# Optimization experiments

Measured on AMD Instinct MI355X. Metric: run time of the kernel, lower is better.

Reference implementation:

```python
import jax, jax.numpy as jnp
import numpy as np

T, B, H, K, V, O, VS, DM = 128, 256, 128, 64, 128, 512, 3, 32


def _ln(x):
    m = jnp.mean(x, -1, keepdims=True)
    v = jnp.var(x, -1, keepdims=True)
    return (x - m) / jnp.sqrt(v + 1e-5)


def setup_inputs() -> dict:
    key = jax.random.key(0)
    ks = jax.random.split(key, 16)
    n = lambda k, shape, std=0.02: jax.random.normal(k, shape, jnp.float32) * std
    return {
        "obs": jax.random.randint(ks[0], (T, B), 0, O),
        "vel": jax.random.normal(ks[1], (T, B, VS), jnp.float32),
        "exploration": jax.random.uniform(ks[2], (T, B), dtype=jnp.float32),
        "hidden_init": n(ks[3], (1, H), 0.5),
        "embed_W": n(ks[4], (O, H)),
        "vel_W": n(ks[5], (H, VS)), "vel_b": jnp.zeros((H,), jnp.float32),
        "hyp_W1": n(ks[6], (DM, VS)), "hyp_b1": jnp.zeros((DM,), jnp.float32),
        "hyp_W2": n(ks[7], (H * H, DM), 0.001), "hyp_b2": jnp.zeros((H * H,), jnp.float32),
        "gate_W": n(ks[8], (H, 2 * H)), "gate_b": jnp.zeros((H,), jnp.float32),
        "pred_W": n(ks[9], (O, H)), "pred_b": jnp.zeros((O,), jnp.float32),
        "mem_W1": n(ks[10], (200, 3)), "mem_b1": jnp.zeros((200,), jnp.float32),
        "mem_W2": n(ks[11], (1, 200)), "mem_b2": jnp.zeros((1,), jnp.float32),
        "Wqk": n(ks[12], (K, H)), "Wv": n(ks[13], (V, H)),
    }


def reference(obs, vel, exploration, hidden_init, embed_W, vel_W, vel_b,
              hyp_W1, hyp_b1, hyp_W2, hyp_b2, gate_W, gate_b, pred_W, pred_b,
              mem_W1, mem_b1, mem_W2, mem_b2, Wqk, Wv):
    i_to_h_all = embed_W[obs]                                       # [T,B,H]
    vel_emb_all = jnp.einsum('tbv,hv->tbh', vel, vel_W) + vel_b      # [T,B,H]
    hyp_h = jax.nn.silu(jnp.einsum('tbv,dv->tbd', vel, hyp_W1) + hyp_b1)  # [T,B,DM]
    h0 = jnp.tanh(jnp.tile(hidden_init, (B, 1)))                     # [B,H]
    keys0 = jnp.zeros((T, B, K), jnp.float32)
    vals0 = jnp.zeros((T, B, V), jnp.float32)
    probs0 = jnp.zeros((T, B), jnp.float32)
    scale = 1.0 / np.sqrt(K).astype(np.float32)

    def step(carry, xs):
        hidden, keys, vals, probs = carry
        i, i_to_h, hyp_t, vemb_t, expl_t = xs
        # hypernet-generated per-sample transition matrix + path integration
        Tm = (hyp_t @ hyp_W2.T + hyp_b2).reshape(B, H, H)
        pi = jnp.einsum('bij,bj->bi', Tm, hidden) + vemb_t
        pi_pred = _ln(jnp.tanh(pi))
        # external-memory dot-product attention over stored (key, value) slots
        q = pi_pred @ Wqk.T                                          # [B,K]
        scores = jnp.einsum('bk,tbk->tb', q, keys) * scale           # [T,B]
        valid = jnp.arange(T)[:, None] < i
        attn = jax.nn.softmax(jnp.where(valid, scores, -1e9), axis=0)
        has_mem = (i > 0).astype(jnp.float32)
        mem_ret = jnp.einsum('tb,tbv->bv', attn * probs, vals) * has_mem
        mem = _ln(mem_ret)
        # sigmoid-gated RNN update between generative (pi) and input paths
        gate = jax.nn.sigmoid(jnp.concatenate([pi, i_to_h], -1) @ gate_W.T + gate_b)
        hidden_new = jnp.tanh(gate * pi + (1.0 - gate) * i_to_h)
        # EM model predicts from the retrieved + normalized memory
        logits = mem @ pred_W.T + pred_b                             # [B,O]
        # write decision MLP on [max inner prod, normalized position, exploration]
        max_ip = jnp.max(jnp.where(valid, scores, -1e9), axis=0) * has_mem
        pos = jnp.full((B,), 1.0, jnp.float32) * (i.astype(jnp.float32) / T)
        feat = jnp.stack([max_ip, pos, expl_t], -1)                  # [B,3]
        h1 = jax.nn.leaky_relu(feat @ mem_W1.T + mem_b1, 0.1)
        p_write = jax.nn.sigmoid(h1 @ mem_W2.T + mem_b2)[:, 0]
        keys = keys.at[i].set(hidden_new @ Wqk.T)
        vals = vals.at[i].set(hidden_new @ Wv.T)
        probs = probs.at[i].set(p_write)
        return (hidden_new, keys, vals, probs), (logits, hidden_new, pi, gate)

    xs = (jnp.arange(T), i_to_h_all, hyp_h, vel_emb_all, exploration)
    _, (logits, inf_h, gen, gating) = jax.lax.scan(step, (h0, keys0, vals0, probs0), xs)
    preds = jax.nn.softmax(logits, axis=-1)
    return preds, logits, inf_h, gen, gating
```

## Files before the change

### kernel.cpp

```cpp
#include <hip/hip_runtime.h>

#ifndef __has_builtin
#define __has_builtin(x) 0
#endif

#define DEV static __device__ __forceinline__

#define TT 128
#define BB 256
#define HH 128
#define KK 64
#define VV 128
#define OO 512
#define JBLK 132
#define KEXT (JBLK*32)

static const size_t PRED_OFF  = 0;
static const size_t LOGIT_OFF = (size_t)TT*BB*OO;
static const size_t INFH_OFF  = LOGIT_OFF + (size_t)TT*BB*OO;
static const size_t GEN_OFF   = INFH_OFF + (size_t)TT*BB*HH;
static const size_t GATE_OFF  = GEN_OFF + (size_t)TT*BB*HH;

typedef float f32x4 __attribute__((ext_vector_type(4)));

DEV unsigned short f2bf(float x){
  unsigned int u = __float_as_uint(x);
  u = (u + 0x7fffu + ((u >> 16) & 1u)) >> 16;
  return (unsigned short)u;
}
DEV float bf2f(unsigned short v){ return __uint_as_float(((unsigned int)v) << 16); }

DEV unsigned char enc8_sw(float x){
  unsigned int u = __float_as_uint(x);
  unsigned int s = (u >> 24) & 0x80u;
  int e = (int)((u >> 23) & 0xffu) - 127;
  unsigned int m = u & 0x7fffffu;
  if (((u >> 23) & 0xffu) == 0) return (unsigned char)s;
  if (e < -10) return (unsigned char)s;
  if (e >= -6) {
    unsigned int mant = m >> 20, rem = m & 0xfffffu;
    if (rem > 0x80000u || (rem == 0x80000u && (mant & 1u))) mant++;
    unsigned int ee = (unsigned int)(e + 7);
    if (mant == 8u) { mant = 0u; ee++; }
    if (ee >= 15u) return (unsigned char)(s | 0x7Eu);
    return (unsigned char)(s | (ee << 3) | mant);
  }
  unsigned int full = 0x800000u | m;
  int sh = 20 + (-6 - e);
  unsigned int mant = full >> sh;
  unsigned int rem  = full & ((1u << sh) - 1u);
  unsigned int halfv = 1u << (sh - 1);
  if (rem > halfv || (rem == halfv && (mant & 1u))) mant++;
  if (mant >= 8u) return (unsigned char)(s | (1u << 3));
  return (unsigned char)(s | mant);
}

DEV unsigned char enc8(float v){
#if __has_builtin(__builtin_amdgcn_cvt_pk_fp8_f32)
  int r = __builtin_amdgcn_cvt_pk_fp8_f32(v, v, 0, false);
  return (unsigned char)(r & 0xff);
#else
  return enc8_sw(v);
#endif
}

DEV unsigned int pack4_fp8(float a, float b, float c, float d){
#if __has_builtin(__builtin_amdgcn_cvt_pk_fp8_f32)
  int w = __builtin_amdgcn_cvt_pk_fp8_f32(a, b, 0, false);
  w = __builtin_amdgcn_cvt_pk_fp8_f32(c, d, w, true);
  return (unsigned int)w;
#else
  return (unsigned int)enc8_sw(a) | ((unsigned int)enc8_sw(b)<<8)
       | ((unsigned int)enc8_sw(c)<<16) | ((unsigned int)enc8_sw(d)<<24);
#endif
}

#define W2_DWORDS 135168
#define GW_DWORDS 8192
__global__ __launch_bounds__(256) void k_pack(const float* __restrict__ hW2,
                                              const float* __restrict__ hb2,
                                              const float* __restrict__ gW,
                                              unsigned char* __restrict__ w2p,
                                              unsigned char* __restrict__ gwp){
  int D = blockIdx.x * 256 + threadIdx.x;
  if (D < W2_DWORDS) {
    int flat = D * 4;
    int l  = (flat >> 3) & 63;
    int w  = (flat >> 9) & 7;
    int j  = flat >> 12;
    int cb = flat & 7;
    int i  = w*16 + (l & 15);
    int db = ((l >> 4) << 3) + cb;
    unsigned int outw = 0;
    for (int cc = 0; cc < 4; ++cc) {
      int d = db + cc;
      float v;
      if (j < 128) v = hW2[((size_t)i*128 + j)*32 + d];
      else         v = hb2[(size_t)i*128 + (j-128)*32 + d];
      outw |= ((unsigned int)enc8(v * 1024.0f)) << (8*cc);
    }
    ((unsigned int*)w2p)[D] = outw;
  } else if (D < W2_DWORDS + GW_DWORDS) {
    int Dg = D - W2_DWORDS;
    int flat = Dg * 4;
    int l  = (flat >> 3) & 63;
    int w  = (flat >> 9) & 7;
    int kc = flat >> 12;
    int cb = flat & 7;
    int i  = w*16 + (l & 15);
    int k0 = kc*32 + ((l >> 4) << 3) + cb;
    unsigned int outw = 0;
    for (int cc = 0; cc < 4; ++cc)
      outw |= ((unsigned int)enc8(gW[(size_t)i*256 + k0 + cc] * 64.0f)) << (8*cc);
    ((unsigned int*)gwp)[Dg] = outw;
  }
}

struct Scan2Smem {
  unsigned long long U[JBLK*64];
  unsigned long long GW[4096];
  float h[128*17];
  float pi[128*17];
  float i2h[128*17];
  float hyps[16*32];
  float velg[64];
  float velWs[384];
  float velbs[128];
  float gbs[128];
  float hypW1s[96];
  float hypb1s[32];
};

__global__ __launch_bounds__(512) void k_scan2(
    const int* __restrict__ obs, const float* __restrict__ vel,
    const float* __restrict__ hinit, const float* __restrict__ embW,
    const float* __restrict__ velW, const float* __restrict__ velb,
    const float* __restrict__ hW1, const float* __restrict__ hb1,
    const float* __restrict__ gb,
    const unsigned char* __restrict__ w2p, const unsigned char* __restrict__ gwp,
    float* __restrict__ out)
{
  extern __shared__ char smemraw[];
  Scan2Smem* sm = (Scan2Smem*)smemraw;
  const int tid = threadIdx.x;
  const int blk = blockIdx.x;
  const int b0 = blk * 16;

  const unsigned long long* gwu = (const unsigned long long*)gwp;
  for (int idx = tid; idx < 4096; idx += 512) sm->GW[idx] = gwu[idx];
  if (tid < 384) sm->velWs[tid] = velW[tid];
  if (tid < 128) { sm->velbs[tid] = velb[tid]; sm->gbs[tid] = gb[tid]; }
  if (tid < 96)  sm->hypW1s[tid] = hW1[tid];
  if (tid < 32)  sm->hypb1s[tid] = hb1[tid];
  if (tid < 128) {
    float hv = tanhf(hinit[tid]);
    #pragma unroll
    for (int g = 0; g < 16; ++g) sm->h[tid*17+g] = hv;
  }
  __syncthreads();

  const int ln = tid & 63, wv = tid >> 6;
  const int gg = tid & 15;
  const int d0 = ((tid >> 4) & 3) << 3;
  const unsigned long long* Au = (const unsigned long long*)w2p + (size_t)wv*64 + ln;

  for (int t = 0; t < TT; ++t) {
    {
      int g2 = tid >> 5, i0 = (tid & 31) << 2;
      int ov = obs[t*BB + b0 + g2];
      float4 e = *(const float4*)&embW[(size_t)ov*HH + i0];
      sm->i2h[(i0+0)*17+g2] = e.x; sm->i2h[(i0+1)*17+g2] = e.y;
      sm->i2h[(i0+2)*17+g2] = e.z; sm->i2h[(i0+3)*17+g2] = e.w;
      int dh = tid & 31;
      const float* vp = &vel[((size_t)t*BB + b0 + g2)*3];
      float a = vp[0]*sm->hypW1s[dh*3+0] + vp[1]*sm->hypW1s[dh*3+1]
              + vp[2]*sm->hypW1s[dh*3+2] + sm->hypb1s[dh];
      sm->hyps[g2*32+dh] = a / (1.0f + __expf(-a));
      if (tid < 48) sm->velg[(tid/3)*4 + tid%3] = vel[((size_t)t*BB + b0 + tid/3)*3 + tid%3];
    }
    __syncthreads();
    {
      float hyp8[8];
      #pragma unroll
      for (int c = 0; c < 8; ++c) hyp8[c] = sm->hyps[gg*32 + d0 + c];
      #pragma unroll
      for (int it = 0; it < 17; ++it) {
        int j = wv + it*8;
        if (j < JBLK) {
          float u[8];
          if (j < 128) {
            float hv = sm->h[j*17+gg] * 32.0f;
            #pragma unroll
            for (int c = 0; c < 8; ++c) u[c] = hv * hyp8[c];
          } else {
            int jj = (j-128)*32 + d0;
            #pragma unroll
            for (int c = 0; c < 8; ++c) u[c] = sm->h[(jj+c)*17+gg] * 32.0f;
          }
          unsigned int w0 = pack4_fp8(u[0], u[1], u[2], u[3]);
          unsigned int w1 = pack4_fp8(u[4], u[5], u[6], u[7]);
          sm->U[j*64 + (tid & 63)] = ((unsigned long long)w1 << 32) | w0;
        }
      }
    }
    __syncthreads();
    {
      f32x4 a0 = {0.f,0.f,0.f,0.f}, a1 = a0, a2 = a0, a3 = a0;
      #pragma unroll 3
      for (int j4 = 0; j4 < JBLK; j4 += 4) {
        long A0 = (long)Au[(size_t)(j4+0)*512]; long B0 = (long)sm->U[(j4+0)*64 + ln];
        long A1 = (long)Au[(size_t)(j4+1)*512]; long B1 = (long)sm->U[(j4+1)*64 + ln];
        long A2 = (long)Au[(size_t)(j4+2)*512]; long B2 = (long)sm->U[(j4+2)*64 + ln];
        long A3 = (long)Au[(size_t)(j4+3)*512]; long B3 = (long)sm->U[(j4+3)*64 + ln];
        a0 = __builtin_amdgcn_mfma_f32_16x16x32_fp8_fp8(A0, B0, a0, 0, 0, 0);
        a1 = __builtin_amdgcn_mfma_f32_16x16x32_fp8_fp8(A1, B1, a1, 0, 0, 0);
        a2 = __builtin_amdgcn_mfma_f32_16x16x32_fp8_fp8(A2, B2, a2, 0, 0, 0);
        a3 = __builtin_amdgcn_mfma_f32_16x16x32_fp8_fp8(A3, B3, a3, 0, 0, 0);
      }
      f32x4 accT = (a0 + a1) + (a2 + a3);
      #pragma unroll
      for (int r = 0; r < 4; ++r) {
        int i = wv*16 + ((ln>>4)<<2) + r, g = ln & 15;
        float p = accT[r] * (1.0f/32768.0f)
                + sm->velg[g*4+0]*sm->velWs[i*3+0] + sm->velg[g*4+1]*sm->velWs[i*3+1]
                + sm->velg[g*4+2]*sm->velWs[i*3+2] + sm->velbs[i];
        sm->pi[i*17+g] = p;
      }
    }
    __syncthreads();
    {
      int kc = tid >> 6;
      int k0 = kc*32 + d0;
      float u[8];
      #pragma unroll
      for (int c = 0; c < 8; ++c) {
        int k = k0 + c;
        u[c] = (k < 128 ? sm->pi[k*17+gg] : sm->i2h[(k-128)*17+gg]) * 32.0f;
      }
      unsigned int w0 = pack4_fp8(u[0], u[1], u[2], u[3]);
      unsigned int w1 = pack4_fp8(u[4], u[5], u[6], u[7]);
      sm->U[kc*64 + (tid & 63)] = ((unsigned long long)w1 << 32) | w0;
    }
    __syncthreads();
    {
      f32x4 ga = {0.f,0.f,0.f,0.f};
      #pragma unroll
      for (int kc = 0; kc < 8; ++kc) {
        long A = (long)sm->GW[(kc*8 + wv)*64 + ln];
        long B = (long)sm->U[kc*64 + ln];
        ga = __builtin_amdgcn_mfma_f32_16x16x32_fp8_fp8(A, B, ga, 0, 0, 0);
      }
      #pragma unroll
      for (int r = 0; r < 4; ++r) {
        int i = wv*16 + ((ln>>4)<<2) + r, g = ln & 15;
        float z = ga[r] * (1.0f/2048.0f) + sm->gbs[i];
        float gt = 1.0f / (1.0f + __expf(-z));
        float pv = sm->pi[i*17+g], ih = sm->i2h[i*17+g];
        float hn = tanhf(gt*pv + (1.0f - gt)*ih);
        sm->h[i*17+g]   = hn;
        sm->i2h[i*17+g] = gt;
      }
    }
    __syncthreads();
    {
      int g2 = tid >> 5, i0 = (tid & 31) << 2;
      size_t ob = ((size_t)t*BB + b0 + g2)*HH + i0;
      float4 v;
      v.x = sm->pi[(i0+0)*17+g2]; v.y = sm->pi[(i0+1)*17+g2];
      v.z = sm->pi[(i0+2)*17+g2]; v.w = sm->pi[(i0+3)*17+g2];
      *(float4*)&out[GEN_OFF + ob] = v;
      v.x = sm->h[(i0+0)*17+g2];  v.y = sm->h[(i0+1)*17+g2];
      v.z = sm->h[(i0+2)*17+g2];  v.w = sm->h[(i0+3)*17+g2];
      *(float4*)&out[INFH_OFF + ob] = v;
      v.x = sm->i2h[(i0+0)*17+g2]; v.y = sm->i2h[(i0+1)*17+g2];
      v.z = sm->i2h[(i0+2)*17+g2]; v.w = sm->i2h[(i0+3)*17+g2];
      *(float4*)&out[GATE_OFF + ob] = v;
    }
    __syncthreads();
  }
}

struct QkvSmem {
  float wqk[64 * 132];
  float wv[128 * 132];
  float pp[132];
  float hh[132];
  float red[4];
  float stats[2];
};

__global__ __launch_bounds__(256) void k_qkv(const float* __restrict__ out,
    const float* __restrict__ Wqk, const float* __restrict__ Wv,
    float* __restrict__ qbuf, unsigned short* __restrict__ keysBF,
    unsigned short* __restrict__ valsBF)
{
  extern __shared__ char smemraw[];
  QkvSmem* sm = (QkvSmem*)smemraw;
  const int tid = threadIdx.x, b = blockIdx.x;

  for (int idx = tid; idx < 64 * 128; idx += 256) { int o = idx >> 7, j = idx & 127; sm->wqk[o * 132 + j] = Wqk[idx]; }
  for (int idx = tid; idx < 128 * 128; idx += 256) { int o = idx >> 7, j = idx & 127; sm->wv[o * 132 + j] = Wv[idx]; }
  __syncthreads();

  for (int t = 0; t < TT; ++t) {
    if (tid < 128) {
      size_t base = ((size_t)t * BB + b) * HH + tid;
      sm->hh[tid] = out[INFH_OFF + base];
      sm->pp[tid] = tanhf(out[GEN_OFF + base]);
    }
    __syncthreads();
    if (tid < 128) {
      float v = sm->pp[tid];
      float s1 = v, s2 = v * v;
      #pragma unroll
      for (int off = 32; off; off >>= 1) { s1 += __shfl_down(s1, off); s2 += __shfl_down(s2, off); }
      if ((tid & 63) == 0) { sm->red[tid >> 6] = s1; sm->red[2 + (tid >> 6)] = s2; }
    }
    __syncthreads();
    if (tid == 0) {
      float s1 = sm->red[0] + sm->red[1], s2 = sm->red[2] + sm->red[3];
      float m = s1 * (1.0f / 128.0f);
      float var = s2 * (1.0f / 128.0f) - m * m;
      sm->stats[0] = m; sm->stats[1] = rsqrtf(var + 1e-5f);
    }
    __syncthreads();
    if (tid < 128) sm->pp[tid] = (sm->pp[tid] - sm->stats[0]) * sm->stats[1];
    __syncthreads();
    {
      int o = tid;
      if (o < 64) {
        const float* wr = &sm->wqk[o * 132];
        float s = 0.f;
        #pragma unroll 8
        for (int j = 0; j < 128; j += 4) {
          float4 xv = *(const float4*)&sm->pp[j];
          float4 w4 = *(const float4*)&wr[j];
          s += xv.x * w4.x + xv.y * w4.y + xv.z * w4.z + xv.w * w4.w;
        }
        qbuf[((size_t)t * BB + b) * KK + o] = s;
      } else if (o < 128) {
        int kk = o - 64;
        const float* wr = &sm->wqk[kk * 132];
        float s = 0.f;
        #pragma unroll 8
        for (int j = 0; j < 128; j += 4) {
          float4 xv = *(const float4*)&sm->hh[j];
          float4 w4 = *(const float4*)&wr[j];
          s += xv.x * w4.x + xv.y * w4.y + xv.z * w4.z + xv.w * w4.w;
        }
        keysBF[((size_t)t * BB + b) * KK + kk] = f2bf(s);
      } else {
        int vv = o - 128;
        const float* wr = &sm->wv[vv * 132];
        float s = 0.f;
        #pragma unroll 8
        for (int j = 0; j < 128; j += 4) {
          float4 xv = *(const float4*)&sm->hh[j];
          float4 w4 = *(const float4*)&wr[j];
          s += xv.x * w4.x + xv.y * w4.y + xv.z * w4.z + xv.w * w4.w;
        }
        valsBF[((size_t)t * BB + b) * VV + vv] = f2bf(s);
      }
    }
    __syncthreads();
  }
}

struct ScoresSmem { float q[128 * 68]; };

__global__ __launch_bounds__(128) void k_scores(const float* __restrict__ qbuf,
    const unsigned short* __restrict__ keysBF, const float* __restrict__ expl,
    const float* __restrict__ mW1, const float* __restrict__ mb1,
    const float* __restrict__ mW2, const float* __restrict__ mb2,
    float* __restrict__ Sg, float* __restrict__ probs)
{
  extern __shared__ char smemraw[];
  ScoresSmem* sm = (ScoresSmem*)smemraw;
  const int tid = threadIdx.x, b = blockIdx.x;

  for (int idx = tid; idx < 128 * 64; idx += 128) {
    int tq = idx >> 6, c = idx & 63;
    sm->q[tq * 68 + c] = qbuf[((size_t)tq * BB + b) * KK + c];
  }
  float kreg[64];
  {
    const uint4* kp = (const uint4*)&keysBF[((size_t)tid * BB + b) * KK];
    #pragma unroll
    for (int qq = 0; qq < 8; ++qq) {
      uint4 kv = kp[qq];
      const unsigned short* ku = (const unsigned short*)&kv;
      #pragma unroll
      for (int c = 0; c < 8; ++c) kreg[qq * 8 + c] = bf2f(ku[c]);
    }
  }
  __syncthreads();

  float* srow = &Sg[(size_t)b * TT * TT];
  for (int tq = 0; tq < TT; ++tq) {
    float s = 0.f;
    #pragma unroll
    for (int c = 0; c < 64; c += 4) {
      float4 qv = *(const float4*)&sm->q[tq * 68 + c];
      s += qv.x * kreg[c] + qv.y * kreg[c + 1] + qv.z * kreg[c + 2] + qv.w * kreg[c + 3];
    }
    srow[(size_t)tq * TT + tid] = s * 0.125f;
  }
  __syncthreads();

  {
    int tq = tid;
    const float* r = &srow[(size_t)tq * TT];
    float mx = -3.0e38f;
    for (int tk = 0; tk < tq; ++tk) mx = fmaxf(mx, r[tk]);
    float f0 = (tq > 0) ? mx : 0.0f;
    float f1 = (float)tq * (1.0f / 128.0f);
    float f2 = expl[(size_t)tq * BB + b];
    float a = 0.f;
    for (int u = 0; u < 200; ++u) {
      float h1 = mW1[u * 3] * f0 + mW1[u * 3 + 1] * f1 + mW1[u * 3 + 2] * f2 + mb1[u];
      h1 = (h1 > 0.f) ? h1 : 0.1f * h1;
      a += mW2[u] * h1;
    }
    float p = 1.0f / (1.0f + __expf(-(a + mb2[0])));
    probs[(size_t)b * TT + tq] = p;
  }
}

struct AttnSmem {
  float w[32 * 132];
  float mem[32 * 132];
  float pw[128 * 132];
};

__global__ __launch_bounds__(256) void k_attn(const float* __restrict__ Sg,
    const float* __restrict__ probs, const unsigned short* __restrict__ valsBF,
    const float* __restrict__ pW, const float* __restrict__ pb,
    float* __restrict__ out)
{
  extern __shared__ char smemraw[];
  AttnSmem* sm = (AttnSmem*)smemraw;
  const int tid = threadIdx.x;
  const int t = blockIdx.x >> 3, g = blockIdx.x & 7;
  const int bloc = tid >> 3, s8 = tid & 7;
  const int b = g * 32 + bloc;

  float acc[16];
  #pragma unroll
  for (int c = 0; c < 16; ++c) acc[c] = 0.f;

  float inv = 0.f;
  if (t > 0) {
    const float* srow = &Sg[((size_t)b * TT + t) * TT];
    float mx = -3.0e38f;
    for (int tk = s8; tk < t; tk += 8) mx = fmaxf(mx, srow[tk]);
    #pragma unroll
    for (int off = 4; off; off >>= 1) mx = fmaxf(mx, __shfl_xor(mx, off, 8));
    float es = 0.f;
    for (int tk = s8; tk < t; tk += 8) {
      float e = __expf(srow[tk] - mx);
      es += e;
      sm->w[bloc * 132 + tk] = e * probs[(size_t)b * TT + tk];
    }
    #pragma unroll
    for (int off = 4; off; off >>= 1) es += __shfl_xor(es, off, 8);
    inv = 1.0f / es;
  }
  __syncthreads();
  if (t > 0) {
    for (int tk = 0; tk < t; ++tk) {
      float wv = sm->w[bloc * 132 + tk] * inv;
      const uint4* vp = (const uint4*)&valsBF[((size_t)tk * BB + b) * VV + s8 * 16];
      uint4 v0 = vp[0], v1 = vp[1];
      const unsigned short* u0 = (const unsigned short*)&v0;
      const unsigned short* u1 = (const unsigned short*)&v1;
      #pragma unroll
      for (int c = 0; c < 8; ++c) acc[c] += wv * bf2f(u0[c]);
      #pragma unroll
      for (int c = 0; c < 8; ++c) acc[8 + c] += wv * bf2f(u1[c]);
    }
  }
  float s1 = 0.f, s2 = 0.f;
  #pragma unroll
  for (int c = 0; c < 16; ++c) { s1 += acc[c]; s2 += acc[c] * acc[c]; }
  #pragma unroll
  for (int off = 4; off; off >>= 1) { s1 += __shfl_xor(s1, off, 8); s2 += __shfl_xor(s2, off, 8); }
  float m = s1 * (1.0f / 128.0f);
  float var = s2 * (1.0f / 128.0f) - m * m;
  float sc = rsqrtf(var + 1e-5f);
  #pragma unroll
  for (int c = 0; c < 16; ++c) sm->mem[bloc * 132 + s8 * 16 + c] = (acc[c] - m) * sc;
  __syncthreads();

  const int og = tid >> 5, bl2 = tid & 31;
  const int b2 = g * 32 + bl2;
  for (int st = 0; st < 4; ++st) {
    for (int idx = tid; idx < 128 * 128; idx += 256) {
      int o = idx >> 7, i = idx & 127;
      sm->pw[o * 132 + i] = pW[((size_t)(st * 128 + o)) * HH + i];
    }
    __syncthreads();
    #pragma unroll
    for (int ob = 0; ob < 4; ++ob) {
      int oo = og * 16 + ob * 4;
      float a0 = pb[st * 128 + oo], a1 = pb[st * 128 + oo + 1];
      float a2 = pb[st * 128 + oo + 2], a3 = pb[st * 128 + oo + 3];
      for (int i = 0; i < 128; i += 4) {
        float4 mv = *(const float4*)&sm->mem[bl2 * 132 + i];
        float4 w0 = *(const float4*)&sm->pw[(oo + 0) * 132 + i];
        float4 w1 = *(const float4*)&sm->pw[(oo + 1) * 132 + i];
        float4 w2 = *(const float4*)&sm->pw[(oo + 2) * 132 + i];
        float4 w3 = *(const float4*)&sm->pw[(oo + 3) * 132 + i];
        a0 += mv.x * w0.x + mv.y * w0.y + mv.z * w0.z + mv.w * w0.w;
        a1 += mv.x * w1.x + mv.y * w1.y + mv.z * w1.z + mv.w * w1.w;
        a2 += mv.x * w2.x + mv.y * w2.y + mv.z * w2.z + mv.w * w2.w;
        a3 += mv.x * w3.x + mv.y * w3.y + mv.z * w3.z + mv.w * w3.w;
      }
      size_t base = LOGIT_OFF + ((size_t)t * BB + b2) * OO + st * 128 + oo;
      out[base] = a0; out[base + 1] = a1; out[base + 2] = a2; out[base + 3] = a3;
    }
    __syncthreads();
  }
  {
    const float* lrow = &out[LOGIT_OFF + ((size_t)t * BB + b) * OO];
    float mx = -3.0e38f;
    for (int o = s8; o < OO; o += 8) mx = fmaxf(mx, lrow[o]);
    #pragma unroll
    for (int off = 4; off; off >>= 1) mx = fmaxf(mx, __shfl_xor(mx, off, 8));
    float zs = 0.f;
    for (int o = s8; o < OO; o += 8) zs += __expf(lrow[o] - mx);
    #pragma unroll
    for (int off = 4; off; off >>= 1) zs += __shfl_xor(zs, off, 8);
    float zi = 1.0f / zs;
    float* prow = &out[PRED_OFF + ((size_t)t * BB + b) * OO];
    for (int o = s8; o < OO; o += 8) prow[o] = __expf(lrow[o] - mx) * zi;
  }
}

extern "C" void kernel_launch(void* const* d_in, const int* in_sizes, int n_in,
                              void* d_out, int out_size, void* d_ws, size_t ws_size,
                              hipStream_t stream) {
  (void)in_sizes; (void)n_in; (void)out_size; (void)ws_size;
  const int*   obs   = (const int*)d_in[0];
  const float* vel   = (const float*)d_in[1];
  const float* expl  = (const float*)d_in[2];
  const float* hinit = (const float*)d_in[3];
  const float* embW  = (const float*)d_in[4];
  const float* velW  = (const float*)d_in[5];
  const float* velb  = (const float*)d_in[6];
  const float* hW1   = (const float*)d_in[7];
  const float* hb1   = (const float*)d_in[8];
  const float* hW2   = (const float*)d_in[9];
  const float* hb2   = (const float*)d_in[10];
  const float* gW    = (const float*)d_in[11];
  const float* gb    = (const float*)d_in[12];
  const float* pW    = (const float*)d_in[13];
  const float* pb    = (const float*)d_in[14];
  const float* mW1   = (const float*)d_in[15];
  const float* mb1   = (const float*)d_in[16];
  const float* mW2   = (const float*)d_in[17];
  const float* mb2   = (const float*)d_in[18];
  const float* Wqk   = (const float*)d_in[19];
  const float* Wv    = (const float*)d_in[20];
  float* out = (float*)d_out;
  char* ws = (char*)d_ws;

  unsigned char*  w2p    = (unsigned char*)(ws + 0);
  unsigned char*  gwp    = (unsigned char*)(ws + 589824);
  float*          qbuf   = (float*)(ws + 1048576);
  unsigned short* keysBF = (unsigned short*)(ws + 9437184);
  unsigned short* valsBF = (unsigned short*)(ws + 13631488);
  float*          Sg     = (float*)(ws + 22020096);
  float*          probs  = (float*)(ws + 38797312);

  k_pack  <<<dim3(560),  dim3(256), 0,                   stream>>>(hW2, hb2, gW, w2p, gwp);
  k_scan2 <<<dim3(16),   dim3(512), sizeof(Scan2Smem),   stream>>>(obs, vel, hinit, embW, velW, velb,
                                                                   hW1, hb1, gb, w2p, gwp, out);
  k_qkv   <<<dim3(256),  dim3(256), sizeof(QkvSmem),     stream>>>(out, Wqk, Wv, qbuf, keysBF, valsBF);
  k_scores<<<dim3(256),  dim3(128), sizeof(ScoresSmem),  stream>>>(qbuf, keysBF, expl, mW1, mb1, mW2, mb2,
                                                                   Sg, probs);
  k_attn  <<<dim3(1024), dim3(256), sizeof(AttnSmem),    stream>>>(Sg, probs, valsBF, pW, pb, out);
}
```

Measured before the change: 3.282 ms.

## Keep hypernet and gate weights resident in registers across scan steps

```diff
diff --git a/kernel.cpp b/kernel.cpp
--- a/kernel.cpp
+++ b/kernel.cpp
@@ -14,6 +14,8 @@
 #define OO 512
 #define JBLK 132
 #define KEXT (JBLK*32)
+#define NJR 64
+#define NSTR (JBLK-NJR)
 
 static const size_t PRED_OFF  = 0;
 static const size_t LOGIT_OFF = (size_t)TT*BB*OO;
@@ -116,9 +118,8 @@
   }
 }
 
-struct Scan2Smem {
+struct Scan3Smem {
   unsigned long long U[JBLK*64];
-  unsigned long long GW[4096];
   float h[128*17];
   float pi[128*17];
   float i2h[128*17];
@@ -131,7 +132,7 @@
   float hypb1s[32];
 };
 
-__global__ __launch_bounds__(512) void k_scan2(
+__global__ __launch_bounds__(512) void k_scan3(
     const int* __restrict__ obs, const float* __restrict__ vel,
     const float* __restrict__ hinit, const float* __restrict__ embW,
     const float* __restrict__ velW, const float* __restrict__ velb,
@@ -141,13 +142,11 @@
     float* __restrict__ out)
 {
   extern __shared__ char smemraw[];
-  Scan2Smem* sm = (Scan2Smem*)smemraw;
+  Scan3Smem* sm = (Scan3Smem*)smemraw;
   const int tid = threadIdx.x;
   const int blk = blockIdx.x;
   const int b0 = blk * 16;
 
-  const unsigned long long* gwu = (const unsigned long long*)gwp;
-  for (int idx = tid; idx < 4096; idx += 512) sm->GW[idx] = gwu[idx];
   if (tid < 384) sm->velWs[tid] = velW[tid];
   if (tid < 128) { sm->velbs[tid] = velb[tid]; sm->gbs[tid] = gb[tid]; }
   if (tid < 96)  sm->hypW1s[tid] = hW1[tid];
@@ -163,6 +162,14 @@
   const int gg = tid & 15;
   const int d0 = ((tid >> 4) & 3) << 3;
   const unsigned long long* Au = (const unsigned long long*)w2p + (size_t)wv*64 + ln;
+  const unsigned long long* Gu = (const unsigned long long*)gwp;
+
+  unsigned long long Areg[NJR];
+  #pragma unroll
+  for (int r = 0; r < NJR; ++r) Areg[r] = Au[(size_t)r*512];
+  unsigned long long GWreg[8];
+  #pragma unroll
+  for (int kc = 0; kc < 8; ++kc) GWreg[kc] = Gu[(size_t)(kc*8 + wv)*64 + ln];
 
   for (int t = 0; t < TT; ++t) {
     {
@@ -205,19 +212,32 @@
     }
     __syncthreads();
     {
-      f32x4 a0 = {0.f,0.f,0.f,0.f}, a1 = a0, a2 = a0, a3 = a0;
-      #pragma unroll 3
-      for (int j4 = 0; j4 < JBLK; j4 += 4) {
-        long A0 = (long)Au[(size_t)(j4+0)*512]; long B0 = (long)sm->U[(j4+0)*64 + ln];
-        long A1 = (long)Au[(size_t)(j4+1)*512]; long B1 = (long)sm->U[(j4+1)*64 + ln];
-        long A2 = (long)Au[(size_t)(j4+2)*512]; long B2 = (long)sm->U[(j4+2)*64 + ln];
-        long A3 = (long)Au[(size_t)(j4+3)*512]; long B3 = (long)sm->U[(j4+3)*64 + ln];
-        a0 = __builtin_amdgcn_mfma_f32_16x16x32_fp8_fp8(A0, B0, a0, 0, 0, 0);
-        a1 = __builtin_amdgcn_mfma_f32_16x16x32_fp8_fp8(A1, B1, a1, 0, 0, 0);
-        a2 = __builtin_amdgcn_mfma_f32_16x16x32_fp8_fp8(A2, B2, a2, 0, 0, 0);
-        a3 = __builtin_amdgcn_mfma_f32_16x16x32_fp8_fp8(A3, B3, a3, 0, 0, 0);
-      }
-      f32x4 accT = (a0 + a1) + (a2 + a3);
+      unsigned long long As[8];
+      #pragma unroll
+      for (int p = 0; p < 8; ++p) As[p] = Au[(size_t)(NJR+p)*512];
+
+      f32x4 acc[4];
+      #pragma unroll
+      for (int r = 0; r < 4; ++r) acc[r] = (f32x4){0.f,0.f,0.f,0.f};
+
+      #pragma unroll
+      for (int j4 = 0; j4 < NJR; j4 += 4) {
+        long B0 = (long)sm->U[(j4+0)*64 + ln];
+        long B1 = (long)sm->U[(j4+1)*64 + ln];
+        long B2 = (long)sm->U[(j4+2)*64 + ln];
+        long B3 = (long)sm->U[(j4+3)*64 + ln];
+        acc[0] = __builtin_amdgcn_mfma_f32_16x16x32_fp8_fp8((long)Areg[j4+0], B0, acc[0], 0, 0, 0);
+        acc[1] = __builtin_amdgcn_mfma_f32_16x16x32_fp8_fp8((long)Areg[j4+1], B1, acc[1], 0, 0, 0);
+        acc[2] = __builtin_amdgcn_mfma_f32_16x16x32_fp8_fp8((long)Areg[j4+2], B2, acc[2], 0, 0, 0);
+        acc[3] = __builtin_amdgcn_mfma_f32_16x16x32_fp8_fp8((long)Areg[j4+3], B3, acc[3], 0, 0, 0);
+      }
+      #pragma unroll
+      for (int c = 0; c < NSTR; ++c) {
+        long B = (long)sm->U[(NJR+c)*64 + ln];
+        acc[c & 3] = __builtin_amdgcn_mfma_f32_16x16x32_fp8_fp8((long)As[c & 7], B, acc[c & 3], 0, 0, 0);
+        if (c + 8 < NSTR) As[c & 7] = Au[(size_t)(NJR+c+8)*512];
+      }
+      f32x4 accT = (acc[0] + acc[1]) + (acc[2] + acc[3]);
       #pragma unroll
       for (int r = 0; r < 4; ++r) {
         int i = wv*16 + ((ln>>4)<<2) + r, g = ln & 15;
@@ -246,9 +266,8 @@
       f32x4 ga = {0.f,0.f,0.f,0.f};
       #pragma unroll
       for (int kc = 0; kc < 8; ++kc) {
-        long A = (long)sm->GW[(kc*8 + wv)*64 + ln];
         long B = (long)sm->U[kc*64 + ln];
-        ga = __builtin_amdgcn_mfma_f32_16x16x32_fp8_fp8(A, B, ga, 0, 0, 0);
+        ga = __builtin_amdgcn_mfma_f32_16x16x32_fp8_fp8((long)GWreg[kc], B, ga, 0, 0, 0);
       }
       #pragma unroll
       for (int r = 0; r < 4; ++r) {
@@ -573,7 +592,7 @@
   float*          probs  = (float*)(ws + 38797312);
 
   k_pack  <<<dim3(560),  dim3(256), 0,                   stream>>>(hW2, hb2, gW, w2p, gwp);
-  k_scan2 <<<dim3(16),   dim3(512), sizeof(Scan2Smem),   stream>>>(obs, vel, hinit, embW, velW, velb,
+  k_scan3 <<<dim3(16),   dim3(512), sizeof(Scan3Smem),   stream>>>(obs, vel, hinit, embW, velW, velb,
                                                                    hW1, hb1, gb, w2p, gwp, out);
   k_qkv   <<<dim3(256),  dim3(256), sizeof(QkvSmem),     stream>>>(out, Wqk, Wv, qbuf, keysBF, valsBF);
   k_scores<<<dim3(256),  dim3(128), sizeof(ScoresSmem),  stream>>>(qbuf, keysBF, expl, mW1, mb1, mW2, mb2,
```

Result: faster. 2.885 ms (-12.1%).
